# Optimization experiments

Hardware: AMD Instinct MI355X
Metric: run time of the kernel (lower is better)

## Reference

```python
import jax, jax.numpy as jnp
from jax import lax
import numpy as np

T, B, H = 128, 4096, 64

def setup_inputs() -> dict:
    key = jax.random.key(0)
    ks = jax.random.split(key, 7)
    s = 1.0 / np.sqrt(H)
    Hseq = jax.random.normal(ks[0], (T, B, H), dtype=jnp.float32)
    # PyTorch nn.GRU params: weight_ih_l0 [3H,H], weight_hh_l0 [3H,H], biases [3H]; gate order r,z,n
    W_ih = jax.random.uniform(ks[1], (3 * H, H), jnp.float32, -s, s)
    W_hh = jax.random.uniform(ks[2], (3 * H, H), jnp.float32, -s, s)
    b_ih = jax.random.uniform(ks[3], (3 * H,), jnp.float32, -s, s)
    b_hh = jax.random.uniform(ks[4], (3 * H,), jnp.float32, -s, s)
    W_out = jax.random.uniform(ks[5], (1, H), jnp.float32, -s, s)
    b_out = jax.random.uniform(ks[6], (1,), jnp.float32, -s, s)
    return {"Hseq": Hseq, "W_ih": W_ih, "W_hh": W_hh, "b_ih": b_ih, "b_hh": b_hh, "W_out": W_out, "b_out": b_out}

def reference(Hseq, W_ih, W_hh, b_ih, b_hh, W_out, b_out):
    # Precompute all input-side gate projections in one big GEMM: [T,B,3H]
    x_gates = jnp.einsum('tbh,gh->tbg', Hseq, W_ih) + b_ih

    def step(h, xg):
        hg = h @ W_hh.T + b_hh                     # [B,3H]
        xr, xz, xn = jnp.split(xg, 3, axis=-1)
        hr, hz, hn = jnp.split(hg, 3, axis=-1)
        r = jax.nn.sigmoid(xr + hr)
        z = jax.nn.sigmoid(xz + hz)
        n = jnp.tanh(xn + r * hn)
        h_new = (1.0 - z) * n + z * h
        return h_new, None

    h0 = jnp.zeros(Hseq.shape[1:], Hseq.dtype)      # [B,H], PyTorch default h0=0
    last, _ = lax.scan(step, h0, x_gates)           # last hidden == Y[-1]
    return (last @ W_out.T + b_out).squeeze(-1)     # [B]
```

## Files before the change

### kernel.cpp

```cpp
#include <hip/hip_runtime.h>
#include <stdint.h>

#define TT 128
#define BB 4096
#define HH 64
#define BC 16
#define XSTR 196
#define HSTR 72

typedef __attribute__((ext_vector_type(8))) short bf16x8;
typedef __attribute__((ext_vector_type(4))) float f32x4;

static __device__ __forceinline__ short f2bf(float f) {
  uint32_t u = __builtin_bit_cast(uint32_t, f);
  u += 0x7fffu + ((u >> 16) & 1u);
  return (short)(u >> 16);
}
static __device__ __forceinline__ uint32_t cvtpk(float a, float b) {
  uint32_t r;
  asm("v_cvt_pk_bf16_f32 %0, %1, %2" : "=v"(r) : "v"(a), "v"(b));
  return r;
}
static __device__ __forceinline__ float rcpf(float x) { return __builtin_amdgcn_rcpf(x); }

static __device__ __forceinline__ void block_sync_lds() {
  asm volatile("" ::: "memory");
  asm volatile("s_waitcnt lgkmcnt(0)" ::: "memory");
  __builtin_amdgcn_s_barrier();
  asm volatile("" ::: "memory");
}

#define MFMA __builtin_amdgcn_mfma_f32_16x16x32_bf16

__global__ __launch_bounds__(512) void gru_fused(
    const float* __restrict__ Hseq, const float* __restrict__ W_ih,
    const float* __restrict__ W_hh, const float* __restrict__ b_ih,
    const float* __restrict__ b_hh, const float* __restrict__ W_out,
    const float* __restrict__ b_out, float* __restrict__ out) {
  __shared__ __align__(16) short hsh[2][BC][HSTR];
  __shared__ __align__(16) float xgsh[2][BC][XSTR];
  __shared__ float psum[4][BC];

  const int tid = threadIdx.x;
  const int w   = tid >> 6;
  const int gw  = w & 3;
  const bool cons = (w < 4);
  const int l   = tid & 63;
  const int llo = l & 15;
  const int lhi = l >> 4;
  const int k0  = lhi * 8;
  const int bbase = blockIdx.x * BC;

  for (int i = tid; i < BC * HSTR; i += 512) ((short*)hsh[0])[i] = 0;

  bf16x8 wa[3][2];
  f32x4 biasHN = {0, 0, 0, 0};
  f32x4 biasPR = {0, 0, 0, 0}, biasPZ = {0, 0, 0, 0}, biasPN = {0, 0, 0, 0};

  if (cons) {
#pragma unroll
    for (int c = 0; c < 3; ++c) {
      const int grow = 16 * gw + 64 * c + llo;
#pragma unroll
      for (int hf = 0; hf < 2; ++hf) {
        const float* q = &W_hh[grow * 64 + hf * 32 + k0];
        bf16x8 b;
#pragma unroll
        for (int i = 0; i < 8; ++i) b[i] = f2bf(q[i]);
        wa[c][hf] = b;
      }
    }
#pragma unroll
    for (int r = 0; r < 4; ++r) biasHN[r] = b_hh[128 + 16 * gw + 4 * lhi + r];
  } else {
#pragma unroll
    for (int c = 0; c < 3; ++c) {
      const int grow = 16 * gw + 64 * c + llo;
#pragma unroll
      for (int hf = 0; hf < 2; ++hf) {
        const float* p = &W_ih[grow * 64 + hf * 32 + k0];
        bf16x8 a;
#pragma unroll
        for (int i = 0; i < 8; ++i) a[i] = f2bf(p[i]);
        wa[c][hf] = a;
      }
    }
#pragma unroll
    for (int r = 0; r < 4; ++r) {
      const int j = 16 * gw + 4 * lhi + r;
      biasPR[r] = b_ih[j] + b_hh[j];
      biasPZ[r] = b_ih[64 + j] + b_hh[64 + j];
      biasPN[r] = b_ih[128 + j];
    }
  }

  const float* xroot = Hseq + (size_t)(bbase + llo) * HH + k0;
  f32x4 xqA0, xqA1, xqA2, xqA3, xqB0, xqB1, xqB2, xqB3;
  f32x4 hfp = {0.f, 0.f, 0.f, 0.f};

  if (!cons) {
    const f32x4* pv = (const f32x4*)xroot;
    f32x4 q0 = pv[0], q1 = pv[1], q2 = pv[8], q3 = pv[9];
    union { uint32_t u[4]; bf16x8 v; } c0, c1;
    c0.u[0] = cvtpk(q0[0], q0[1]); c0.u[1] = cvtpk(q0[2], q0[3]);
    c0.u[2] = cvtpk(q1[0], q1[1]); c0.u[3] = cvtpk(q1[2], q1[3]);
    c1.u[0] = cvtpk(q2[0], q2[1]); c1.u[1] = cvtpk(q2[2], q2[3]);
    c1.u[2] = cvtpk(q3[0], q3[1]); c1.u[3] = cvtpk(q3[2], q3[3]);
    f32x4 cR = biasPR, cZ = biasPZ, cN = biasPN;
    cR = MFMA(wa[0][0], c0.v, cR, 0, 0, 0);
    cR = MFMA(wa[0][1], c1.v, cR, 0, 0, 0);
    cZ = MFMA(wa[1][0], c0.v, cZ, 0, 0, 0);
    cZ = MFMA(wa[1][1], c1.v, cZ, 0, 0, 0);
    cN = MFMA(wa[2][0], c0.v, cN, 0, 0, 0);
    cN = MFMA(wa[2][1], c1.v, cN, 0, 0, 0);
    *(f32x4*)&xgsh[0][llo][16 * gw + 4 * lhi]       = cR;
    *(f32x4*)&xgsh[0][llo][64 + 16 * gw + 4 * lhi]  = cZ;
    *(f32x4*)&xgsh[0][llo][128 + 16 * gw + 4 * lhi] = cN;
    const f32x4* pa = (const f32x4*)(xroot + (size_t)1 * BB * HH);
    xqA0 = pa[0]; xqA1 = pa[1]; xqA2 = pa[8]; xqA3 = pa[9];
    const f32x4* pb = (const f32x4*)(xroot + (size_t)2 * BB * HH);
    xqB0 = pb[0]; xqB1 = pb[1]; xqB2 = pb[8]; xqB3 = pb[9];
  }
  block_sync_lds();

#define CSTEP(RB, WB)                                                         \
  {                                                                           \
    __builtin_amdgcn_s_setprio(1);                                            \
    const bf16x8 hb0 = *(const bf16x8*)&hsh[RB][llo][k0];                     \
    const bf16x8 hb1 = *(const bf16x8*)&hsh[RB][llo][k0 + 32];                \
    f32x4 aR = *(const f32x4*)&xgsh[RB][llo][16 * gw + 4 * lhi];              \
    aR = MFMA(wa[0][0], hb0, aR, 0, 0, 0);                                    \
    aR = MFMA(wa[0][1], hb1, aR, 0, 0, 0);                                    \
    f32x4 aZ  = *(const f32x4*)&xgsh[RB][llo][64 + 16 * gw + 4 * lhi];        \
    f32x4 aXN = *(const f32x4*)&xgsh[RB][llo][128 + 16 * gw + 4 * lhi];       \
    aZ  = MFMA(wa[1][0], hb0, aZ, 0, 0, 0);                                   \
    aZ  = MFMA(wa[1][1], hb1, aZ, 0, 0, 0);                                   \
    f32x4 aHN = MFMA(wa[2][0], hb0, biasHN, 0, 0, 0);                         \
    aHN = MFMA(wa[2][1], hb1, aHN, 0, 0, 0);                                  \
    _Pragma("unroll")                                                         \
    for (int r = 0; r < 4; ++r) {                                             \
      const float u  = __expf(-aR[r]);                                        \
      const float az = fminf(30.f, fmaxf(-30.f, aZ[r]));                      \
      const float t  = __expf(-az);                                           \
      const float rr = rcpf(1.0f + u);                                        \
      float c = aXN[r] + rr * aHN[r];                                         \
      c = fminf(15.f, fmaxf(-15.f, c));                                       \
      const float s   = __expf(2.0f * c);                                     \
      const float qq  = s + 1.0f;                                             \
      const float num = t * (s - 1.0f) + hfp[r] * qq;                         \
      const float den = qq * (1.0f + t);                                      \
      hfp[r] = num * rcpf(den);                                               \
    }                                                                         \
    uint2 pk;                                                                 \
    pk.x = cvtpk(hfp[0], hfp[1]);                                             \
    pk.y = cvtpk(hfp[2], hfp[3]);                                             \
    *(uint2*)&hsh[WB][llo][16 * gw + 4 * lhi] = pk;                           \
    __builtin_amdgcn_s_setprio(0);                                            \
  }

#define PSTEP(OB, XQ0, XQ1, XQ2, XQ3, TN)                                     \
  {                                                                           \
    union { uint32_t u[4]; bf16x8 v; } c0, c1;                                \
    c0.u[0] = cvtpk(XQ0[0], XQ0[1]); c0.u[1] = cvtpk(XQ0[2], XQ0[3]);         \
    c0.u[2] = cvtpk(XQ1[0], XQ1[1]); c0.u[3] = cvtpk(XQ1[2], XQ1[3]);         \
    c1.u[0] = cvtpk(XQ2[0], XQ2[1]); c1.u[1] = cvtpk(XQ2[2], XQ2[3]);         \
    c1.u[2] = cvtpk(XQ3[0], XQ3[1]); c1.u[3] = cvtpk(XQ3[2], XQ3[3]);         \
    {                                                                         \
      const int tn = (TN) < TT ? (TN) : (TT - 1);                             \
      const f32x4* pv = (const f32x4*)(xroot + (size_t)tn * BB * HH);         \
      XQ0 = pv[0]; XQ1 = pv[1]; XQ2 = pv[8]; XQ3 = pv[9];                     \
    }                                                                         \
    f32x4 cR = biasPR, cZ = biasPZ, cN = biasPN;                              \
    cR = MFMA(wa[0][0], c0.v, cR, 0, 0, 0);                                   \
    cR = MFMA(wa[0][1], c1.v, cR, 0, 0, 0);                                   \
    cZ = MFMA(wa[1][0], c0.v, cZ, 0, 0, 0);                                   \
    cZ = MFMA(wa[1][1], c1.v, cZ, 0, 0, 0);                                   \
    cN = MFMA(wa[2][0], c0.v, cN, 0, 0, 0);                                   \
    cN = MFMA(wa[2][1], c1.v, cN, 0, 0, 0);                                   \
    *(f32x4*)&xgsh[OB][llo][16 * gw + 4 * lhi]       = cR;                    \
    *(f32x4*)&xgsh[OB][llo][64 + 16 * gw + 4 * lhi]  = cZ;                    \
    *(f32x4*)&xgsh[OB][llo][128 + 16 * gw + 4 * lhi] = cN;                    \
  }

  for (int t = 0; t < TT; t += 2) {
    if (cons) { CSTEP(0, 1) } else { PSTEP(1, xqA0, xqA1, xqA2, xqA3, t + 3) }
    block_sync_lds();
    if (cons) { CSTEP(1, 0) } else { PSTEP(0, xqB0, xqB1, xqB2, xqB3, t + 4) }
    block_sync_lds();
  }
#undef CSTEP
#undef PSTEP

  if (cons) {
    float part = 0.f;
#pragma unroll
    for (int r = 0; r < 4; ++r) part += hfp[r] * W_out[16 * gw + 4 * lhi + r];
    part += __shfl_xor(part, 16);
    part += __shfl_xor(part, 32);
    if (lhi == 0) psum[gw][llo] = part;
  }
  block_sync_lds();
  if (tid < BC)
    out[bbase + tid] = psum[0][tid] + psum[1][tid] + psum[2][tid] + psum[3][tid] + b_out[0];
}

extern "C" void kernel_launch(void* const* d_in, const int* in_sizes, int n_in,
                              void* d_out, int out_size, void* d_ws, size_t ws_size,
                              hipStream_t stream) {
  (void)in_sizes; (void)n_in; (void)d_ws; (void)ws_size; (void)out_size;
  const float* Hseq  = (const float*)d_in[0];
  const float* W_ih  = (const float*)d_in[1];
  const float* W_hh  = (const float*)d_in[2];
  const float* b_ih  = (const float*)d_in[3];
  const float* b_hh  = (const float*)d_in[4];
  const float* W_out = (const float*)d_in[5];
  const float* b_out = (const float*)d_in[6];
  float* out = (float*)d_out;
  gru_fused<<<BB / BC, 512, 0, stream>>>(Hseq, W_ih, W_hh, b_ih, b_hh, W_out, b_out, out);
}
```

Measured before the change: 70.72 us.

## Deepen xgate buffering to four stages and prefetch next step's gates into registers

The producer warps now compute input-gate projections two steps ahead into a 4-deep LDS ring, and consumer warps load the next step's x-gates into registers during the current step. This takes the LDS read latency off the recurrent critical path. The R-gate MFMA chain is split into two independent accumulations that are summed, and the gate math is simplified to plain sigmoid/tanh helpers without clamping. The setprio hints are removed. The costs are more LDS and registers, and the unclamped exp could overflow to inf for large inputs.

```diff
diff --git a/kernel.cpp b/kernel.cpp
--- a/kernel.cpp
+++ b/kernel.cpp
@@ -22,6 +22,11 @@
   return r;
 }
 static __device__ __forceinline__ float rcpf(float x) { return __builtin_amdgcn_rcpf(x); }
+static __device__ __forceinline__ float sigm(float x) { return rcpf(1.0f + __expf(-x)); }
+static __device__ __forceinline__ float tanhf_fast(float x) {
+  float e = __expf(2.0f * x);
+  return 1.0f - 2.0f * rcpf(e + 1.0f);
+}
 
 static __device__ __forceinline__ void block_sync_lds() {
   asm volatile("" ::: "memory");
@@ -38,7 +43,7 @@
     const float* __restrict__ b_hh, const float* __restrict__ W_out,
     const float* __restrict__ b_out, float* __restrict__ out) {
   __shared__ __align__(16) short hsh[2][BC][HSTR];
-  __shared__ __align__(16) float xgsh[2][BC][XSTR];
+  __shared__ __align__(16) float xgsh[4][BC][XSTR];
   __shared__ float psum[4][BC];
 
   const int tid = threadIdx.x;
@@ -50,12 +55,13 @@
   const int lhi = l >> 4;
   const int k0  = lhi * 8;
   const int bbase = blockIdx.x * BC;
+  const f32x4 fz = {0.f, 0.f, 0.f, 0.f};
 
   for (int i = tid; i < BC * HSTR; i += 512) ((short*)hsh[0])[i] = 0;
 
   bf16x8 wa[3][2];
-  f32x4 biasHN = {0, 0, 0, 0};
-  f32x4 biasPR = {0, 0, 0, 0}, biasPZ = {0, 0, 0, 0}, biasPN = {0, 0, 0, 0};
+  f32x4 biasHN = fz;
+  f32x4 biasPR = fz, biasPZ = fz, biasPN = fz;
 
   if (cons) {
 #pragma unroll
@@ -96,69 +102,71 @@
 
   const float* xroot = Hseq + (size_t)(bbase + llo) * HH + k0;
   f32x4 xqA0, xqA1, xqA2, xqA3, xqB0, xqB1, xqB2, xqB3;
-  f32x4 hfp = {0.f, 0.f, 0.f, 0.f};
+  f32x4 hfp = fz;
+  f32x4 xgE0, xgE1, xgE2, xgO0, xgO1, xgO2;
 
   if (!cons) {
-    const f32x4* pv = (const f32x4*)xroot;
-    f32x4 q0 = pv[0], q1 = pv[1], q2 = pv[8], q3 = pv[9];
-    union { uint32_t u[4]; bf16x8 v; } c0, c1;
-    c0.u[0] = cvtpk(q0[0], q0[1]); c0.u[1] = cvtpk(q0[2], q0[3]);
-    c0.u[2] = cvtpk(q1[0], q1[1]); c0.u[3] = cvtpk(q1[2], q1[3]);
-    c1.u[0] = cvtpk(q2[0], q2[1]); c1.u[1] = cvtpk(q2[2], q2[3]);
-    c1.u[2] = cvtpk(q3[0], q3[1]); c1.u[3] = cvtpk(q3[2], q3[3]);
-    f32x4 cR = biasPR, cZ = biasPZ, cN = biasPN;
-    cR = MFMA(wa[0][0], c0.v, cR, 0, 0, 0);
-    cR = MFMA(wa[0][1], c1.v, cR, 0, 0, 0);
-    cZ = MFMA(wa[1][0], c0.v, cZ, 0, 0, 0);
-    cZ = MFMA(wa[1][1], c1.v, cZ, 0, 0, 0);
-    cN = MFMA(wa[2][0], c0.v, cN, 0, 0, 0);
-    cN = MFMA(wa[2][1], c1.v, cN, 0, 0, 0);
-    *(f32x4*)&xgsh[0][llo][16 * gw + 4 * lhi]       = cR;
-    *(f32x4*)&xgsh[0][llo][64 + 16 * gw + 4 * lhi]  = cZ;
-    *(f32x4*)&xgsh[0][llo][128 + 16 * gw + 4 * lhi] = cN;
-    const f32x4* pa = (const f32x4*)(xroot + (size_t)1 * BB * HH);
+#pragma unroll
+    for (int s = 0; s < 2; ++s) {
+      const f32x4* pv = (const f32x4*)(xroot + (size_t)s * BB * HH);
+      f32x4 q0 = pv[0], q1 = pv[1], q2 = pv[8], q3 = pv[9];
+      union { uint32_t u[4]; bf16x8 v; } c0, c1;
+      c0.u[0] = cvtpk(q0[0], q0[1]); c0.u[1] = cvtpk(q0[2], q0[3]);
+      c0.u[2] = cvtpk(q1[0], q1[1]); c0.u[3] = cvtpk(q1[2], q1[3]);
+      c1.u[0] = cvtpk(q2[0], q2[1]); c1.u[1] = cvtpk(q2[2], q2[3]);
+      c1.u[2] = cvtpk(q3[0], q3[1]); c1.u[3] = cvtpk(q3[2], q3[3]);
+      f32x4 cR = biasPR, cZ = biasPZ, cN = biasPN;
+      cR = MFMA(wa[0][0], c0.v, cR, 0, 0, 0);
+      cR = MFMA(wa[0][1], c1.v, cR, 0, 0, 0);
+      cZ = MFMA(wa[1][0], c0.v, cZ, 0, 0, 0);
+      cZ = MFMA(wa[1][1], c1.v, cZ, 0, 0, 0);
+      cN = MFMA(wa[2][0], c0.v, cN, 0, 0, 0);
+      cN = MFMA(wa[2][1], c1.v, cN, 0, 0, 0);
+      *(f32x4*)&xgsh[s][llo][16 * gw + 4 * lhi]       = cR;
+      *(f32x4*)&xgsh[s][llo][64 + 16 * gw + 4 * lhi]  = cZ;
+      *(f32x4*)&xgsh[s][llo][128 + 16 * gw + 4 * lhi] = cN;
+    }
+    const f32x4* pa = (const f32x4*)(xroot + (size_t)2 * BB * HH);
     xqA0 = pa[0]; xqA1 = pa[1]; xqA2 = pa[8]; xqA3 = pa[9];
-    const f32x4* pb = (const f32x4*)(xroot + (size_t)2 * BB * HH);
+    const f32x4* pb = (const f32x4*)(xroot + (size_t)3 * BB * HH);
     xqB0 = pb[0]; xqB1 = pb[1]; xqB2 = pb[8]; xqB3 = pb[9];
   }
   block_sync_lds();
 
-#define CSTEP(RB, WB)                                                         \
+  if (cons) {
+    xgE0 = *(const f32x4*)&xgsh[0][llo][16 * gw + 4 * lhi];
+    xgE1 = *(const f32x4*)&xgsh[0][llo][64 + 16 * gw + 4 * lhi];
+    xgE2 = *(const f32x4*)&xgsh[0][llo][128 + 16 * gw + 4 * lhi];
+  }
+
+#define CSTEP(RBH, WBH, NB, XGC0, XGC1, XGC2, XGN0, XGN1, XGN2)               \
   {                                                                           \
-    __builtin_amdgcn_s_setprio(1);                                            \
-    const bf16x8 hb0 = *(const bf16x8*)&hsh[RB][llo][k0];                     \
-    const bf16x8 hb1 = *(const bf16x8*)&hsh[RB][llo][k0 + 32];                \
-    f32x4 aR = *(const f32x4*)&xgsh[RB][llo][16 * gw + 4 * lhi];              \
-    aR = MFMA(wa[0][0], hb0, aR, 0, 0, 0);                                    \
-    aR = MFMA(wa[0][1], hb1, aR, 0, 0, 0);                                    \
-    f32x4 aZ  = *(const f32x4*)&xgsh[RB][llo][64 + 16 * gw + 4 * lhi];        \
-    f32x4 aXN = *(const f32x4*)&xgsh[RB][llo][128 + 16 * gw + 4 * lhi];       \
-    aZ  = MFMA(wa[1][0], hb0, aZ, 0, 0, 0);                                   \
-    aZ  = MFMA(wa[1][1], hb1, aZ, 0, 0, 0);                                   \
+    const bf16x8 hb0 = *(const bf16x8*)&hsh[RBH][llo][k0];                    \
+    const bf16x8 hb1 = *(const bf16x8*)&hsh[RBH][llo][k0 + 32];               \
+    XGN0 = *(const f32x4*)&xgsh[NB][llo][16 * gw + 4 * lhi];                  \
+    XGN1 = *(const f32x4*)&xgsh[NB][llo][64 + 16 * gw + 4 * lhi];             \
+    XGN2 = *(const f32x4*)&xgsh[NB][llo][128 + 16 * gw + 4 * lhi];            \
+    f32x4 aR0 = MFMA(wa[0][0], hb0, XGC0, 0, 0, 0);                           \
+    f32x4 aR1 = MFMA(wa[0][1], hb1, fz, 0, 0, 0);                             \
+    f32x4 aZ  = MFMA(wa[1][0], hb0, XGC1, 0, 0, 0);                           \
+    aZ        = MFMA(wa[1][1], hb1, aZ, 0, 0, 0);                             \
     f32x4 aHN = MFMA(wa[2][0], hb0, biasHN, 0, 0, 0);                         \
-    aHN = MFMA(wa[2][1], hb1, aHN, 0, 0, 0);                                  \
+    aHN       = MFMA(wa[2][1], hb1, aHN, 0, 0, 0);                            \
+    const f32x4 aR = aR0 + aR1;                                               \
     _Pragma("unroll")                                                         \
     for (int r = 0; r < 4; ++r) {                                             \
-      const float u  = __expf(-aR[r]);                                        \
-      const float az = fminf(30.f, fmaxf(-30.f, aZ[r]));                      \
-      const float t  = __expf(-az);                                           \
-      const float rr = rcpf(1.0f + u);                                        \
-      float c = aXN[r] + rr * aHN[r];                                         \
-      c = fminf(15.f, fmaxf(-15.f, c));                                       \
-      const float s   = __expf(2.0f * c);                                     \
-      const float qq  = s + 1.0f;                                             \
-      const float num = t * (s - 1.0f) + hfp[r] * qq;                         \
-      const float den = qq * (1.0f + t);                                      \
-      hfp[r] = num * rcpf(den);                                               \
+      const float rr = sigm(aR[r]);                                           \
+      const float zz = sigm(aZ[r]);                                           \
+      const float nn = tanhf_fast(XGC2[r] + rr * aHN[r]);                     \
+      hfp[r] = nn + zz * (hfp[r] - nn);                                       \
     }                                                                         \
     uint2 pk;                                                                 \
     pk.x = cvtpk(hfp[0], hfp[1]);                                             \
     pk.y = cvtpk(hfp[2], hfp[3]);                                             \
-    *(uint2*)&hsh[WB][llo][16 * gw + 4 * lhi] = pk;                           \
-    __builtin_amdgcn_s_setprio(0);                                            \
-  }
-
-#define PSTEP(OB, XQ0, XQ1, XQ2, XQ3, TN)                                     \
+    *(uint2*)&hsh[WBH][llo][16 * gw + 4 * lhi] = pk;                          \
+  }
+
+#define PSTEP(WRBUF, XQ0, XQ1, XQ2, XQ3, TN)                                  \
   {                                                                           \
     union { uint32_t u[4]; bf16x8 v; } c0, c1;                                \
     c0.u[0] = cvtpk(XQ0[0], XQ0[1]); c0.u[1] = cvtpk(XQ0[2], XQ0[3]);         \
@@ -177,15 +185,23 @@
     cZ = MFMA(wa[1][1], c1.v, cZ, 0, 0, 0);                                   \
     cN = MFMA(wa[2][0], c0.v, cN, 0, 0, 0);                                   \
     cN = MFMA(wa[2][1], c1.v, cN, 0, 0, 0);                                   \
-    *(f32x4*)&xgsh[OB][llo][16 * gw + 4 * lhi]       = cR;                    \
-    *(f32x4*)&xgsh[OB][llo][64 + 16 * gw + 4 * lhi]  = cZ;                    \
-    *(f32x4*)&xgsh[OB][llo][128 + 16 * gw + 4 * lhi] = cN;                    \
-  }
-
-  for (int t = 0; t < TT; t += 2) {
-    if (cons) { CSTEP(0, 1) } else { PSTEP(1, xqA0, xqA1, xqA2, xqA3, t + 3) }
-    block_sync_lds();
-    if (cons) { CSTEP(1, 0) } else { PSTEP(0, xqB0, xqB1, xqB2, xqB3, t + 4) }
+    *(f32x4*)&xgsh[WRBUF][llo][16 * gw + 4 * lhi]       = cR;                 \
+    *(f32x4*)&xgsh[WRBUF][llo][64 + 16 * gw + 4 * lhi]  = cZ;                 \
+    *(f32x4*)&xgsh[WRBUF][llo][128 + 16 * gw + 4 * lhi] = cN;                 \
+  }
+
+  for (int t = 0; t < TT; t += 4) {
+    if (cons) { CSTEP(0, 1, 1, xgE0, xgE1, xgE2, xgO0, xgO1, xgO2) }
+    else      { PSTEP(2, xqA0, xqA1, xqA2, xqA3, t + 4) }
+    block_sync_lds();
+    if (cons) { CSTEP(1, 0, 2, xgO0, xgO1, xgO2, xgE0, xgE1, xgE2) }
+    else      { PSTEP(3, xqB0, xqB1, xqB2, xqB3, t + 5) }
+    block_sync_lds();
+    if (cons) { CSTEP(0, 1, 3, xgE0, xgE1, xgE2, xgO0, xgO1, xgO2) }
+    else      { PSTEP(0, xqA0, xqA1, xqA2, xqA3, t + 6) }
+    block_sync_lds();
+    if (cons) { CSTEP(1, 0, 0, xgO0, xgO1, xgO2, xgE0, xgE1, xgE2) }
+    else      { PSTEP(1, xqB0, xqB1, xqB2, xqB3, t + 7) }
     block_sync_lds();
   }
 #undef CSTEP
```

Result: no change. 69.72 us (-1.4%).
